# Performance work log

Hardware: AMD Instinct MI355X
Metric: run time of the kernel (lower is better)

Reference implementation:

```python
import jax, jax.numpy as jnp
import numpy as np

N_NODES = 50000
N_EDGES = 800000
N_GRAPHS = 512
IN_DIM, HID_DIM, LAT_DIM = 128, 128, 64


def _glorot(key, fan_in, fan_out):
    lim = np.sqrt(6.0 / (fan_in + fan_out))
    return jax.random.uniform(key, (fan_in, fan_out), jnp.float32, -lim, lim)


def gcn_conv(x, W, b, src, dst, deg_inv_sqrt):
    """PyG GCNConv: out = D^{-1/2}(A+I)D^{-1/2} x W + b (self-loops included)."""
    h = x @ W  # [N, F_out]
    norm = deg_inv_sqrt[src] * deg_inv_sqrt[dst]  # [E]
    msg = h[src] * norm[:, None]  # gather + scale, [E, F_out]
    out = jax.ops.segment_sum(msg, dst, num_segments=x.shape[0])  # scatter-add
    out = out + h * (deg_inv_sqrt * deg_inv_sqrt)[:, None]  # self-loop term
    return out + b


def setup_inputs() -> dict:
    key = jax.random.key(0)
    ks = jax.random.split(key, 12)
    x = jax.random.normal(ks[0], (N_NODES, IN_DIM), jnp.float32)
    edge_index = jax.random.randint(ks[1], (2, N_EDGES), 0, N_NODES, jnp.int64)
    batch = jnp.sort(jax.random.randint(ks[2], (N_NODES,), 0, N_GRAPHS, jnp.int64))
    return {
        "x": x,
        "edge_index": edge_index,
        "batch": batch,
        "W1": _glorot(ks[3], IN_DIM, HID_DIM), "b1": jnp.zeros((HID_DIM,), jnp.float32),
        "W2": _glorot(ks[4], HID_DIM, LAT_DIM), "b2": jnp.zeros((LAT_DIM,), jnp.float32),
        "W3": _glorot(ks[5], LAT_DIM, HID_DIM), "b3": jnp.zeros((HID_DIM,), jnp.float32),
        "W4": _glorot(ks[6], HID_DIM, IN_DIM), "b4": jnp.zeros((IN_DIM,), jnp.float32),
    }


def reference(x, edge_index, batch, W1, b1, W2, b2, W3, b3, W4, b4):
    n = x.shape[0]
    src, dst = edge_index[0], edge_index[1]
    # degrees with self-loops (PyG computes deg over col=dst, +1 for self-loop)
    deg = jax.ops.segment_sum(jnp.ones_like(dst, dtype=x.dtype), dst, num_segments=n) + 1.0
    dis = jax.lax.rsqrt(deg)
    # encoder
    h = jax.nn.relu(gcn_conv(x, W1, b1, src, dst, dis))
    z = gcn_conv(h, W2, b2, src, dst, dis)
    # scatter-mean pooling over graphs
    counts = jax.ops.segment_sum(jnp.ones((n,), x.dtype), batch, num_segments=N_GRAPHS)
    agg = jax.ops.segment_sum(z, batch, num_segments=N_GRAPHS) / jnp.maximum(counts, 1.0)[:, None]
    # decoder
    h2 = jax.nn.relu(gcn_conv(z, W3, b3, src, dst, dis))
    x_hat = gcn_conv(h2, W4, b4, src, dst, dis)
    return (x_hat, z, agg)
```

## Files before the change

### kernel.cpp

```cpp
#include <hip/hip_runtime.h>
#include <hip/hip_fp16.h>
#include <math.h>

#define N_NODES 50000
#define N_EDGES 800000
#define N_GRAPHS 512
#define CAP 62
#define NBINS 196
#define CAPB 5120
#define ABLK 1024

typedef unsigned short u16;
typedef unsigned int u32;
typedef __attribute__((ext_vector_type(8))) short bf16x8_t;
typedef __attribute__((ext_vector_type(4))) float f32x4_t;

constexpr int NBLK_A = (N_EDGES + ABLK - 1) / ABLK;

__device__ __forceinline__ u16 f2bf(float f) {
    u32 u = __builtin_bit_cast(u32, f);
    return (u16)((u + 0x7fffu + ((u >> 16) & 1u)) >> 16);
}
__device__ __forceinline__ float bf2f(u16 s) {
    return __builtin_bit_cast(float, (u32)s << 16);
}
__device__ __forceinline__ float bf_lo(u32 u) { return __builtin_bit_cast(float, u << 16); }
__device__ __forceinline__ float bf_hi(u32 u) { return __builtin_bit_cast(float, u & 0xffff0000u); }

__device__ __forceinline__ int block_exscan(int val, int* lds, int tid) {
    lds[tid] = val;
    __syncthreads();
#pragma unroll
    for (int off = 1; off < 256; off <<= 1) {
        int t = (tid >= off) ? lds[tid - off] : 0;
        __syncthreads();
        lds[tid] += t;
        __syncthreads();
    }
    return lds[tid] - val;
}

__global__ __launch_bounds__(256) void bin_scatter(const int* __restrict__ src,
                                                   const int* __restrict__ dst,
                                                   u32* __restrict__ binCnt,
                                                   u32* __restrict__ binList) {
    __shared__ int cur[NBINS];
    __shared__ int lsStart[NBINS];
    __shared__ int gbase[NBINS];
    __shared__ int scanbuf[256];
    __shared__ u32 stage[ABLK];
    __shared__ int gpos[ABLK];
    int t = threadIdx.x;
    int e0 = blockIdx.x * ABLK;
    int nEdge = min(ABLK, N_EDGES - e0);

    for (int i = t; i < NBINS; i += 256) cur[i] = 0;
    __syncthreads();

    int myBin[4], myRank[4];
    u32 myPack[4];
    int nmy = 0;
    if (t * 4 < nEdge) {
        nmy = 4;
        int4 dv = *reinterpret_cast<const int4*>(dst + e0 + t * 4);
        int4 sv = *reinterpret_cast<const int4*>(src + e0 + t * 4);
        int ds[4] = {dv.x, dv.y, dv.z, dv.w};
        int ss[4] = {sv.x, sv.y, sv.z, sv.w};
#pragma unroll
        for (int j = 0; j < 4; j++) {
            int d = ds[j];
            int bin = d >> 8;
            myBin[j] = bin;
            myPack[j] = (u32)(ss[j] & 0xFFFF) | ((u32)(d & 0xFF) << 16);
            myRank[j] = atomicAdd(&cur[bin], 1);
        }
    }
    __syncthreads();
    int v = (t < NBINS) ? cur[t] : 0;
    int ex = block_exscan(v, scanbuf, t);
    if (t < NBINS) {
        lsStart[t] = ex;
        gbase[t] = (v > 0) ? (int)atomicAdd(&binCnt[t * 16], (u32)v) : 0;
    }
    __syncthreads();
    for (int j = 0; j < nmy; j++) {
        int bin = myBin[j];
        int idx = lsStart[bin] + myRank[j];
        int p = gbase[bin] + myRank[j];
        stage[idx] = myPack[j];
        gpos[idx] = (p < CAPB) ? (bin * CAPB + p) : -1;
    }
    __syncthreads();
    for (int i = t; i < nEdge; i += 256) {
        int p = gpos[i];
        if (p >= 0) binList[p] = stage[i];
    }
}

__global__ __launch_bounds__(256) void bucket_build(const u32* __restrict__ binList,
                                                    const u32* __restrict__ binCnt,
                                                    u32* __restrict__ bucket,
                                                    float* __restrict__ dis) {
    __shared__ u32 rec[256 * 32];
    int b = blockIdx.x, t = threadIdx.x;
    for (int i = t; i < 256 * 32; i += 256) rec[i] = 0;
    __syncthreads();
    int ecnt = min((int)binCnt[b * 16], CAPB);
    const u32* lst = binList + (size_t)b * CAPB;
    u16* rec16 = reinterpret_cast<u16*>(rec);
    for (int i = t; i < ecnt; i += 256) {
        u32 pk = lst[i];
        int dlow = (pk >> 16) & 0xFF;
        int pos = (int)atomicAdd(&rec[dlow * 32], 1u);
        if (pos < CAP) rec16[dlow * 64 + 2 + pos] = (u16)(pk & 0xFFFF);
    }
    __syncthreads();
    int node0 = b * 256;
    int nNode = min(256, N_NODES - node0);
    for (int i = t; i < nNode * 32; i += 256)
        bucket[(size_t)node0 * 32 + i] = rec[i];
    if (t < nNode) dis[node0 + t] = 1.0f / sqrtf((float)rec[t * 32] + 1.0f);
}

__global__ void convert_x_bf16(const float* __restrict__ x, u16* __restrict__ xb) {
    int i = blockIdx.x * 256 + threadIdx.x;
    if (i >= (N_NODES * 128) / 4) return;
    float4 v = reinterpret_cast<const float4*>(x)[i];
    u32 lo = (u32)f2bf(v.x) | ((u32)f2bf(v.y) << 16);
    u32 hi = (u32)f2bf(v.z) | ((u32)f2bf(v.w) << 16);
    reinterpret_cast<uint2*>(xb)[i] = make_uint2(lo, hi);
}

__global__ void convert_wT_all(const float* __restrict__ W1, u16* __restrict__ wt1,
                               const float* __restrict__ W2, u16* __restrict__ wt2,
                               const float* __restrict__ W3, u16* __restrict__ wt3,
                               const float* __restrict__ W4, u16* __restrict__ wt4) {
    int idx = blockIdx.x * 256 + threadIdx.x;
    const float* Wf;
    u16* Wt;
    int K, N, off;
    if (idx < 16384)      { Wf = W1; Wt = wt1; K = 128; N = 128; off = 0; }
    else if (idx < 24576) { Wf = W2; Wt = wt2; K = 128; N = 64;  off = 16384; }
    else if (idx < 32768) { Wf = W3; Wt = wt3; K = 64;  N = 128; off = 24576; }
    else if (idx < 49152) { Wf = W4; Wt = wt4; K = 128; N = 128; off = 32768; }
    else return;
    int t = idx - off;
    int k = t / N, n = t % N;
    Wt[n * K + k] = f2bf(Wf[t]);
}

template <int N, int K, bool BIAS, bool RELU, bool SCALE>
__global__ __launch_bounds__(256) void gemm_mfma(const u16* __restrict__ A,
                                                 const u16* __restrict__ Wt,
                                                 const float* __restrict__ bias,
                                                 const float* __restrict__ dis,
                                                 u16* __restrict__ C) {
    constexpr int KB = K / 32;
    constexpr int TN = N / 64;
    constexpr int TM = (N_NODES + 63) / 64;
    int wave = threadIdx.x >> 6;
    int lane = threadIdx.x & 63;
    int W = blockIdx.x * 4 + wave;
    if (W >= TM * TN) return;
    int tm = W / TN, tn = W % TN;
    int r16 = lane & 15;
    int kg = lane >> 4;

    bf16x8_t bf[4][KB];
#pragma unroll
    for (int nr = 0; nr < 4; nr++) {
        int colg = tn * 64 + nr * 16 + r16;
#pragma unroll
        for (int kb = 0; kb < KB; kb++)
            bf[nr][kb] = *reinterpret_cast<const bf16x8_t*>(Wt + (size_t)colg * K + kb * 32 + kg * 8);
    }

    f32x4_t acc[4][4];
#pragma unroll
    for (int mr = 0; mr < 4; mr++)
#pragma unroll
        for (int nr = 0; nr < 4; nr++)
#pragma unroll
            for (int t = 0; t < 4; t++) acc[mr][nr][t] = 0.f;

#pragma unroll
    for (int mr = 0; mr < 4; mr++) {
        int row = tm * 64 + mr * 16 + r16;
        if (row >= N_NODES) row = N_NODES - 1;
        bf16x8_t af[KB];
#pragma unroll
        for (int kb = 0; kb < KB; kb++)
            af[kb] = *reinterpret_cast<const bf16x8_t*>(A + (size_t)row * K + kb * 32 + kg * 8);
#pragma unroll
        for (int kb = 0; kb < KB; kb++)
#pragma unroll
            for (int nr = 0; nr < 4; nr++)
                acc[mr][nr] = __builtin_amdgcn_mfma_f32_16x16x32_bf16(af[kb], bf[nr][kb],
                                                                      acc[mr][nr], 0, 0, 0);
    }

#pragma unroll
    for (int mr = 0; mr < 4; mr++) {
        float sc[4];
#pragma unroll
        for (int r = 0; r < 4; r++) {
            int row = tm * 64 + mr * 16 + kg * 4 + r;
            sc[r] = (SCALE && row < N_NODES) ? dis[row] : 1.f;
        }
#pragma unroll
        for (int nr = 0; nr < 4; nr++) {
            int colg = tn * 64 + nr * 16 + r16;
            float bv = BIAS ? bias[colg] : 0.f;
#pragma unroll
            for (int r = 0; r < 4; r++) {
                int row = tm * 64 + mr * 16 + kg * 4 + r;
                if (row < N_NODES) {
                    float v = acc[mr][nr][r] + bv;
                    if (RELU) v = fmaxf(v, 0.f);
                    if (SCALE) v *= sc[r];
                    C[(size_t)row * N + colg] = f2bf(v);
                }
            }
        }
    }
}

template <int F, bool RELU, bool BIAS, bool WF32, bool WBF16, bool SCALEOUT>
__global__ __launch_bounds__(256) void propagate_b(const u16* __restrict__ h,
                                                   const u32* __restrict__ bucket,
                                                   const float* __restrict__ dis,
                                                   const float* __restrict__ bias,
                                                   float* __restrict__ out_f,
                                                   u16* __restrict__ out_b) {
    int w = (blockIdx.x * blockDim.x + threadIdx.x) >> 6;
    int lane = threadIdx.x & 63;
    if (w >= N_NODES) return;
    const u32* bw = bucket + (size_t)w * 32;
    int deg = __builtin_amdgcn_readfirstlane(min((int)bw[0], CAP));
    const u16* slots = reinterpret_cast<const u16*>(bw) + 2;
    const u32* sw = reinterpret_cast<const u32*>(reinterpret_cast<const char*>(bw) + 4);
    float di = dis[w];

    if (F == 128) {
        const u32* hw = reinterpret_cast<const u32*>(h);
        float2 a0 = {0.f, 0.f}, a1 = {0.f, 0.f}, a2 = {0.f, 0.f}, a3 = {0.f, 0.f};
        int i = 0;
        for (; i + 16 <= deg; i += 16) {
            u32 cw[8], hv[16];
#pragma unroll
            for (int j = 0; j < 8; j++) cw[j] = sw[(i >> 1) + j];
#pragma unroll
            for (int j = 0; j < 8; j++) {
                hv[2 * j]     = hw[(size_t)(cw[j] & 0xffffu) * 64 + lane];
                hv[2 * j + 1] = hw[(size_t)(cw[j] >> 16) * 64 + lane];
            }
#pragma unroll
            for (int j = 0; j < 16; j++) {
                float lo = bf_lo(hv[j]), hi = bf_hi(hv[j]);
                if ((j & 3) == 0) { a0.x += lo; a0.y += hi; }
                else if ((j & 3) == 1) { a1.x += lo; a1.y += hi; }
                else if ((j & 3) == 2) { a2.x += lo; a2.y += hi; }
                else { a3.x += lo; a3.y += hi; }
            }
        }
        for (; i + 8 <= deg; i += 8) {
            u32 cw[4], hv[8];
#pragma unroll
            for (int j = 0; j < 4; j++) cw[j] = sw[(i >> 1) + j];
#pragma unroll
            for (int j = 0; j < 4; j++) {
                hv[2 * j]     = hw[(size_t)(cw[j] & 0xffffu) * 64 + lane];
                hv[2 * j + 1] = hw[(size_t)(cw[j] >> 16) * 64 + lane];
            }
#pragma unroll
            for (int j = 0; j < 8; j++) {
                float lo = bf_lo(hv[j]), hi = bf_hi(hv[j]);
                if ((j & 3) == 0) { a0.x += lo; a0.y += hi; }
                else if ((j & 3) == 1) { a1.x += lo; a1.y += hi; }
                else if ((j & 3) == 2) { a2.x += lo; a2.y += hi; }
                else { a3.x += lo; a3.y += hi; }
            }
        }
        for (; i < deg; i++) {
            u32 u = hw[(size_t)slots[i] * 64 + lane];
            a0.x += bf_lo(u);
            a0.y += bf_hi(u);
        }
        u32 su = hw[(size_t)w * 64 + lane];
        float ox = (a0.x + a1.x + a2.x + a3.x + bf_lo(su)) * di;
        float oy = (a0.y + a1.y + a2.y + a3.y + bf_hi(su)) * di;
        if (BIAS) {
            float2 bv = reinterpret_cast<const float2*>(bias)[lane];
            ox += bv.x;
            oy += bv.y;
        }
        if (RELU) { ox = fmaxf(ox, 0.f); oy = fmaxf(oy, 0.f); }
        if (WF32) {
            reinterpret_cast<float2*>(out_f + (size_t)w * 128)[lane] = make_float2(ox, oy);
        }
        if (WBF16) {
            float wx = SCALEOUT ? ox * di : ox;
            float wy = SCALEOUT ? oy * di : oy;
            u32 pk = (u32)f2bf(wx) | ((u32)f2bf(wy) << 16);
            reinterpret_cast<u32*>(out_b)[(size_t)w * 64 + lane] = pk;
        }
    } else {
        float a0 = 0.f, a1 = 0.f, a2 = 0.f, a3 = 0.f;
        int i = 0;
        for (; i + 16 <= deg; i += 16) {
            u32 cw[8];
            u16 hv[16];
#pragma unroll
            for (int j = 0; j < 8; j++) cw[j] = sw[(i >> 1) + j];
#pragma unroll
            for (int j = 0; j < 8; j++) {
                hv[2 * j]     = h[(size_t)(cw[j] & 0xffffu) * 64 + lane];
                hv[2 * j + 1] = h[(size_t)(cw[j] >> 16) * 64 + lane];
            }
#pragma unroll
            for (int j = 0; j < 16; j++) {
                float v = bf2f(hv[j]);
                if ((j & 3) == 0) a0 += v;
                else if ((j & 3) == 1) a1 += v;
                else if ((j & 3) == 2) a2 += v;
                else a3 += v;
            }
        }
        for (; i + 8 <= deg; i += 8) {
            u32 cw[4];
            u16 hv[8];
#pragma unroll
            for (int j = 0; j < 4; j++) cw[j] = sw[(i >> 1) + j];
#pragma unroll
            for (int j = 0; j < 4; j++) {
                hv[2 * j]     = h[(size_t)(cw[j] & 0xffffu) * 64 + lane];
                hv[2 * j + 1] = h[(size_t)(cw[j] >> 16) * 64 + lane];
            }
#pragma unroll
            for (int j = 0; j < 8; j++) {
                float v = bf2f(hv[j]);
                if ((j & 3) == 0) a0 += v;
                else if ((j & 3) == 1) a1 += v;
                else if ((j & 3) == 2) a2 += v;
                else a3 += v;
            }
        }
        for (; i < deg; i++) a0 += bf2f(h[(size_t)slots[i] * 64 + lane]);
        float o = (a0 + a1 + a2 + a3 + bf2f(h[(size_t)w * 64 + lane])) * di;
        if (BIAS) o += bias[lane];
        if (RELU) o = fmaxf(o, 0.f);
        if (WF32) out_f[(size_t)w * 64 + lane] = o;
        if (WBF16) out_b[(size_t)w * 64 + lane] = f2bf(SCALEOUT ? o * di : o);
    }
}

__global__ __launch_bounds__(256) void pool_kernel(const float* __restrict__ z,
                                                   const int* __restrict__ batch,
                                                   float* __restrict__ agg) {
    __shared__ float part[3][64];
    int g = blockIdx.x;
    int wave = threadIdx.x >> 6;
    int lane = threadIdx.x & 63;
    int l = 0, h = N_NODES;
    while (l < h) { int m = (l + h) >> 1; if (batch[m] < g) l = m + 1; else h = m; }
    int s = l;
    h = N_NODES;
    while (l < h) { int m = (l + h) >> 1; if (batch[m] < g + 1) l = m + 1; else h = m; }
    int e = l;
    float acc = 0.f;
    for (int i = s + wave; i < e; i += 4) acc += z[(size_t)i * 64 + lane];
    if (wave) part[wave - 1][lane] = acc;
    __syncthreads();
    if (wave == 0) {
        acc += part[0][lane] + part[1][lane] + part[2][lane];
        agg[(size_t)g * 64 + lane] = acc / fmaxf((float)(e - s), 1.0f);
    }
}

extern "C" void kernel_launch(void* const* d_in, const int* in_sizes, int n_in,
                              void* d_out, int out_size, void* d_ws, size_t ws_size,
                              hipStream_t stream) {
    const float* x   = (const float*)d_in[0];
    const int* eidx  = (const int*)d_in[1];
    const int* batch = (const int*)d_in[2];
    const float* W1  = (const float*)d_in[3];
    const float* b1  = (const float*)d_in[4];
    const float* W2  = (const float*)d_in[5];
    const float* b2  = (const float*)d_in[6];
    const float* W3  = (const float*)d_in[7];
    const float* b3  = (const float*)d_in[8];
    const float* W4  = (const float*)d_in[9];
    const float* b4  = (const float*)d_in[10];

    const int* src = eidx;
    const int* dst = eidx + N_EDGES;

    float* out_xhat = (float*)d_out;
    float* out_z    = out_xhat + (size_t)N_NODES * 128;
    float* out_agg  = out_z + (size_t)N_NODES * 64;

    char* p = (char*)d_ws;
    auto alloc = [&](size_t bytes) { char* r = p; p += (bytes + 255) & ~(size_t)255; return r; };
    u16* arena0 = (u16*)alloc((size_t)N_NODES * 128 * 2);
    u16* arena1 = (u16*)alloc((size_t)N_NODES * 128 * 2);
    u16* c1     = (u16*)alloc((size_t)N_NODES * 64 * 2);
    u16* c2     = (u16*)alloc((size_t)N_NODES * 64 * 2);
    u16* wt1    = (u16*)alloc(128 * 128 * 2);
    u16* wt2    = (u16*)alloc(128 * 64 * 2);
    u16* wt3    = (u16*)alloc(64 * 128 * 2);
    u16* wt4    = (u16*)alloc(128 * 128 * 2);
    u32* bucket = (u32*)alloc((size_t)N_NODES * 128);
    u32* binCnt = (u32*)alloc(NBINS * 16 * 4);
    u32* binList= (u32*)alloc((size_t)NBINS * CAPB * 4);
    float* dis  = (float*)alloc(N_NODES * 4);

    hipMemsetAsync(binCnt, 0, NBINS * 16 * 4, stream);
    bin_scatter<<<NBLK_A, 256, 0, stream>>>(src, dst, binCnt, binList);
    bucket_build<<<NBINS, 256, 0, stream>>>(binList, binCnt, bucket, dis);

    convert_x_bf16<<<(N_NODES * 128 / 4 + 255) / 256, 256, 0, stream>>>(x, arena0);
    convert_wT_all<<<(49152 + 255) / 256, 256, 0, stream>>>(W1, wt1, W2, wt2, W3, wt3, W4, wt4);

    const int PROP_GRID = (N_NODES + 3) / 4;
    const int G128 = ((N_NODES + 63) / 64 * 2 + 3) / 4;
    const int G64  = ((N_NODES + 63) / 64 * 1 + 3) / 4;

    gemm_mfma<128, 128, false, false, true><<<G128, 256, 0, stream>>>(arena0, wt1, nullptr, dis, arena1);
    propagate_b<128, true, true, false, true, false><<<PROP_GRID, 256, 0, stream>>>(
        arena1, bucket, dis, b1, nullptr, arena0);
    gemm_mfma<64, 128, false, false, true><<<G64, 256, 0, stream>>>(arena0, wt2, nullptr, dis, c1);
    propagate_b<64, false, true, true, true, true><<<PROP_GRID, 256, 0, stream>>>(
        c1, bucket, dis, b2, out_z, c2);
    pool_kernel<<<N_GRAPHS, 256, 0, stream>>>(out_z, batch, out_agg);
    propagate_b<64, false, false, false, true, false><<<PROP_GRID, 256, 0, stream>>>(
        c2, bucket, dis, nullptr, nullptr, c1);
    gemm_mfma<128, 64, true, true, false><<<G128, 256, 0, stream>>>(c1, wt3, b3, dis, arena1);
    gemm_mfma<128, 128, false, false, true><<<G128, 256, 0, stream>>>(arena1, wt4, nullptr, dis, arena0);
    propagate_b<128, false, true, true, false, false><<<PROP_GRID, 256, 0, stream>>>(
        arena0, bucket, dis, b4, out_xhat, nullptr);
}
```

Measured before the change: 267.0 us.

## Fuse x conversion into first GEMM, merge weight conversion, persistent propagate grid

Removes the separate fp32-to-bf16 conversion kernel for x by having the first GEMM load fp32 rows and convert them in registers. The weight-transpose conversion moves into extra blocks of the edge-binning kernel, saving a launch. The propagate kernels switch to a fixed grid of 2048 blocks with a grid-stride loop over nodes, and the bias load is hoisted out of that loop. This cuts launches and one full pass over x. The cost is that the first GEMM now reads twice as many bytes, and the fixed grid may balance load unevenly across nodes.

```diff
diff --git a/kernel.cpp b/kernel.cpp
--- a/kernel.cpp
+++ b/kernel.cpp
@@ -9,13 +9,17 @@
 #define NBINS 196
 #define CAPB 5120
 #define ABLK 1024
+#define PROP_BLOCKS 2048
+#define PROP_WAVES (PROP_BLOCKS * 4)
 
 typedef unsigned short u16;
 typedef unsigned int u32;
 typedef __attribute__((ext_vector_type(8))) short bf16x8_t;
 typedef __attribute__((ext_vector_type(4))) float f32x4_t;
+typedef __attribute__((ext_vector_type(4))) unsigned int u32x4_t;
 
 constexpr int NBLK_A = (N_EDGES + ABLK - 1) / ABLK;
+constexpr int NCW = (49152 + 255) / 256;
 
 __device__ __forceinline__ u16 f2bf(float f) {
     u32 u = __builtin_bit_cast(u32, f);
@@ -26,6 +30,17 @@
 }
 __device__ __forceinline__ float bf_lo(u32 u) { return __builtin_bit_cast(float, u << 16); }
 __device__ __forceinline__ float bf_hi(u32 u) { return __builtin_bit_cast(float, u & 0xffff0000u); }
+
+__device__ __forceinline__ bf16x8_t cvt8(const float* p) {
+    float4 a = *reinterpret_cast<const float4*>(p);
+    float4 b = *reinterpret_cast<const float4*>(p + 4);
+    u32x4_t w;
+    w.x = (u32)f2bf(a.x) | ((u32)f2bf(a.y) << 16);
+    w.y = (u32)f2bf(a.z) | ((u32)f2bf(a.w) << 16);
+    w.z = (u32)f2bf(b.x) | ((u32)f2bf(b.y) << 16);
+    w.w = (u32)f2bf(b.z) | ((u32)f2bf(b.w) << 16);
+    return __builtin_bit_cast(bf16x8_t, w);
+}
 
 __device__ __forceinline__ int block_exscan(int val, int* lds, int tid) {
     lds[tid] = val;
@@ -40,10 +55,14 @@
     return lds[tid] - val;
 }
 
-__global__ __launch_bounds__(256) void bin_scatter(const int* __restrict__ src,
+__global__ __launch_bounds__(256) void pre_scatter(const int* __restrict__ src,
                                                    const int* __restrict__ dst,
                                                    u32* __restrict__ binCnt,
-                                                   u32* __restrict__ binList) {
+                                                   u32* __restrict__ binList,
+                                                   const float* __restrict__ W1, u16* __restrict__ wt1,
+                                                   const float* __restrict__ W2, u16* __restrict__ wt2,
+                                                   const float* __restrict__ W3, u16* __restrict__ wt3,
+                                                   const float* __restrict__ W4, u16* __restrict__ wt4) {
     __shared__ int cur[NBINS];
     __shared__ int lsStart[NBINS];
     __shared__ int gbase[NBINS];
@@ -51,6 +70,20 @@
     __shared__ u32 stage[ABLK];
     __shared__ int gpos[ABLK];
     int t = threadIdx.x;
+    if (blockIdx.x >= NBLK_A) {
+        int idx = (blockIdx.x - NBLK_A) * 256 + t;
+        const float* Wf;
+        u16* Wt;
+        int K, N, off;
+        if (idx < 16384)      { Wf = W1; Wt = wt1; K = 128; N = 128; off = 0; }
+        else if (idx < 24576) { Wf = W2; Wt = wt2; K = 128; N = 64;  off = 16384; }
+        else if (idx < 32768) { Wf = W3; Wt = wt3; K = 64;  N = 128; off = 24576; }
+        else                  { Wf = W4; Wt = wt4; K = 128; N = 128; off = 32768; }
+        int q = idx - off;
+        int k = q / N, n = q % N;
+        Wt[n * K + k] = f2bf(Wf[q]);
+        return;
+    }
     int e0 = blockIdx.x * ABLK;
     int nEdge = min(ABLK, N_EDGES - e0);
 
@@ -122,35 +155,8 @@
     if (t < nNode) dis[node0 + t] = 1.0f / sqrtf((float)rec[t * 32] + 1.0f);
 }
 
-__global__ void convert_x_bf16(const float* __restrict__ x, u16* __restrict__ xb) {
-    int i = blockIdx.x * 256 + threadIdx.x;
-    if (i >= (N_NODES * 128) / 4) return;
-    float4 v = reinterpret_cast<const float4*>(x)[i];
-    u32 lo = (u32)f2bf(v.x) | ((u32)f2bf(v.y) << 16);
-    u32 hi = (u32)f2bf(v.z) | ((u32)f2bf(v.w) << 16);
-    reinterpret_cast<uint2*>(xb)[i] = make_uint2(lo, hi);
-}
-
-__global__ void convert_wT_all(const float* __restrict__ W1, u16* __restrict__ wt1,
-                               const float* __restrict__ W2, u16* __restrict__ wt2,
-                               const float* __restrict__ W3, u16* __restrict__ wt3,
-                               const float* __restrict__ W4, u16* __restrict__ wt4) {
-    int idx = blockIdx.x * 256 + threadIdx.x;
-    const float* Wf;
-    u16* Wt;
-    int K, N, off;
-    if (idx < 16384)      { Wf = W1; Wt = wt1; K = 128; N = 128; off = 0; }
-    else if (idx < 24576) { Wf = W2; Wt = wt2; K = 128; N = 64;  off = 16384; }
-    else if (idx < 32768) { Wf = W3; Wt = wt3; K = 64;  N = 128; off = 24576; }
-    else if (idx < 49152) { Wf = W4; Wt = wt4; K = 128; N = 128; off = 32768; }
-    else return;
-    int t = idx - off;
-    int k = t / N, n = t % N;
-    Wt[n * K + k] = f2bf(Wf[t]);
-}
-
-template <int N, int K, bool BIAS, bool RELU, bool SCALE>
-__global__ __launch_bounds__(256) void gemm_mfma(const u16* __restrict__ A,
+template <int N, int K, bool BIAS, bool RELU, bool SCALE, bool AF32>
+__global__ __launch_bounds__(256) void gemm_mfma(const void* __restrict__ Avp,
                                                  const u16* __restrict__ Wt,
                                                  const float* __restrict__ bias,
                                                  const float* __restrict__ dis,
@@ -189,8 +195,15 @@
         if (row >= N_NODES) row = N_NODES - 1;
         bf16x8_t af[KB];
 #pragma unroll
-        for (int kb = 0; kb < KB; kb++)
-            af[kb] = *reinterpret_cast<const bf16x8_t*>(A + (size_t)row * K + kb * 32 + kg * 8);
+        for (int kb = 0; kb < KB; kb++) {
+            if constexpr (AF32) {
+                const float* Af = (const float*)Avp;
+                af[kb] = cvt8(Af + (size_t)row * K + kb * 32 + kg * 8);
+            } else {
+                const u16* Ab = (const u16*)Avp;
+                af[kb] = *reinterpret_cast<const bf16x8_t*>(Ab + (size_t)row * K + kb * 32 + kg * 8);
+            }
+        }
 #pragma unroll
         for (int kb = 0; kb < KB; kb++)
 #pragma unroll
@@ -232,125 +245,128 @@
                                                    const float* __restrict__ bias,
                                                    float* __restrict__ out_f,
                                                    u16* __restrict__ out_b) {
-    int w = (blockIdx.x * blockDim.x + threadIdx.x) >> 6;
+    int wid = (blockIdx.x * 256 + threadIdx.x) >> 6;
     int lane = threadIdx.x & 63;
-    if (w >= N_NODES) return;
-    const u32* bw = bucket + (size_t)w * 32;
-    int deg = __builtin_amdgcn_readfirstlane(min((int)bw[0], CAP));
-    const u16* slots = reinterpret_cast<const u16*>(bw) + 2;
-    const u32* sw = reinterpret_cast<const u32*>(reinterpret_cast<const char*>(bw) + 4);
-    float di = dis[w];
-
-    if (F == 128) {
-        const u32* hw = reinterpret_cast<const u32*>(h);
-        float2 a0 = {0.f, 0.f}, a1 = {0.f, 0.f}, a2 = {0.f, 0.f}, a3 = {0.f, 0.f};
-        int i = 0;
-        for (; i + 16 <= deg; i += 16) {
-            u32 cw[8], hv[16];
-#pragma unroll
-            for (int j = 0; j < 8; j++) cw[j] = sw[(i >> 1) + j];
-#pragma unroll
-            for (int j = 0; j < 8; j++) {
-                hv[2 * j]     = hw[(size_t)(cw[j] & 0xffffu) * 64 + lane];
-                hv[2 * j + 1] = hw[(size_t)(cw[j] >> 16) * 64 + lane];
-            }
-#pragma unroll
-            for (int j = 0; j < 16; j++) {
-                float lo = bf_lo(hv[j]), hi = bf_hi(hv[j]);
-                if ((j & 3) == 0) { a0.x += lo; a0.y += hi; }
-                else if ((j & 3) == 1) { a1.x += lo; a1.y += hi; }
-                else if ((j & 3) == 2) { a2.x += lo; a2.y += hi; }
-                else { a3.x += lo; a3.y += hi; }
-            }
+    float2 bv2 = make_float2(0.f, 0.f);
+    float bv1 = 0.f;
+    if (BIAS) {
+        if (F == 128) bv2 = reinterpret_cast<const float2*>(bias)[lane];
+        else          bv1 = bias[lane];
+    }
+    for (int w = wid; w < N_NODES; w += PROP_WAVES) {
+        const u32* bw = bucket + (size_t)w * 32;
+        int deg = __builtin_amdgcn_readfirstlane(min((int)bw[0], CAP));
+        const u16* slots = reinterpret_cast<const u16*>(bw) + 2;
+        const u32* sw = reinterpret_cast<const u32*>(reinterpret_cast<const char*>(bw) + 4);
+        float di = dis[w];
+
+        if (F == 128) {
+            const u32* hw = reinterpret_cast<const u32*>(h);
+            float2 a0 = {0.f, 0.f}, a1 = {0.f, 0.f}, a2 = {0.f, 0.f}, a3 = {0.f, 0.f};
+            int i = 0;
+            for (; i + 16 <= deg; i += 16) {
+                u32 cw[8], hv[16];
+#pragma unroll
+                for (int j = 0; j < 8; j++) cw[j] = sw[(i >> 1) + j];
+#pragma unroll
+                for (int j = 0; j < 8; j++) {
+                    hv[2 * j]     = hw[(size_t)(cw[j] & 0xffffu) * 64 + lane];
+                    hv[2 * j + 1] = hw[(size_t)(cw[j] >> 16) * 64 + lane];
+                }
+#pragma unroll
+                for (int j = 0; j < 16; j++) {
+                    float lo = bf_lo(hv[j]), hi = bf_hi(hv[j]);
+                    if ((j & 3) == 0) { a0.x += lo; a0.y += hi; }
+                    else if ((j & 3) == 1) { a1.x += lo; a1.y += hi; }
+                    else if ((j & 3) == 2) { a2.x += lo; a2.y += hi; }
+                    else { a3.x += lo; a3.y += hi; }
+                }
+            }
+            for (; i + 8 <= deg; i += 8) {
+                u32 cw[4], hv[8];
+#pragma unroll
+                for (int j = 0; j < 4; j++) cw[j] = sw[(i >> 1) + j];
+#pragma unroll
+                for (int j = 0; j < 4; j++) {
+                    hv[2 * j]     = hw[(size_t)(cw[j] & 0xffffu) * 64 + lane];
+                    hv[2 * j + 1] = hw[(size_t)(cw[j] >> 16) * 64 + lane];
+                }
+#pragma unroll
+                for (int j = 0; j < 8; j++) {
+                    float lo = bf_lo(hv[j]), hi = bf_hi(hv[j]);
+                    if ((j & 3) == 0) { a0.x += lo; a0.y += hi; }
+                    else if ((j & 3) == 1) { a1.x += lo; a1.y += hi; }
+                    else if ((j & 3) == 2) { a2.x += lo; a2.y += hi; }
+                    else { a3.x += lo; a3.y += hi; }
+                }
+            }
+            for (; i < deg; i++) {
+                u32 u = hw[(size_t)slots[i] * 64 + lane];
+                a0.x += bf_lo(u);
+                a0.y += bf_hi(u);
+            }
+            u32 su = hw[(size_t)w * 64 + lane];
+            float ox = (a0.x + a1.x + a2.x + a3.x + bf_lo(su)) * di;
+            float oy = (a0.y + a1.y + a2.y + a3.y + bf_hi(su)) * di;
+            if (BIAS) { ox += bv2.x; oy += bv2.y; }
+            if (RELU) { ox = fmaxf(ox, 0.f); oy = fmaxf(oy, 0.f); }
+            if (WF32) {
+                reinterpret_cast<float2*>(out_f + (size_t)w * 128)[lane] = make_float2(ox, oy);
+            }
+            if (WBF16) {
+                float wx = SCALEOUT ? ox * di : ox;
+                float wy = SCALEOUT ? oy * di : oy;
+                u32 pk = (u32)f2bf(wx) | ((u32)f2bf(wy) << 16);
+                reinterpret_cast<u32*>(out_b)[(size_t)w * 64 + lane] = pk;
+            }
+        } else {
+            float a0 = 0.f, a1 = 0.f, a2 = 0.f, a3 = 0.f;
+            int i = 0;
+            for (; i + 16 <= deg; i += 16) {
+                u32 cw[8];
+                u16 hv[16];
+#pragma unroll
+                for (int j = 0; j < 8; j++) cw[j] = sw[(i >> 1) + j];
+#pragma unroll
+                for (int j = 0; j < 8; j++) {
+                    hv[2 * j]     = h[(size_t)(cw[j] & 0xffffu) * 64 + lane];
+                    hv[2 * j + 1] = h[(size_t)(cw[j] >> 16) * 64 + lane];
+                }
+#pragma unroll
+                for (int j = 0; j < 16; j++) {
+                    float v = bf2f(hv[j]);
+                    if ((j & 3) == 0) a0 += v;
+                    else if ((j & 3) == 1) a1 += v;
+                    else if ((j & 3) == 2) a2 += v;
+                    else a3 += v;
+                }
+            }
+            for (; i + 8 <= deg; i += 8) {
+                u32 cw[4];
+                u16 hv[8];
+#pragma unroll
+                for (int j = 0; j < 4; j++) cw[j] = sw[(i >> 1) + j];
+#pragma unroll
+                for (int j = 0; j < 4; j++) {
+                    hv[2 * j]     = h[(size_t)(cw[j] & 0xffffu) * 64 + lane];
+                    hv[2 * j + 1] = h[(size_t)(cw[j] >> 16) * 64 + lane];
+                }
+#pragma unroll
+                for (int j = 0; j < 8; j++) {
+                    float v = bf2f(hv[j]);
+                    if ((j & 3) == 0) a0 += v;
+                    else if ((j & 3) == 1) a1 += v;
+                    else if ((j & 3) == 2) a2 += v;
+                    else a3 += v;
+                }
+            }
+            for (; i < deg; i++) a0 += bf2f(h[(size_t)slots[i] * 64 + lane]);
+            float o = (a0 + a1 + a2 + a3 + bf2f(h[(size_t)w * 64 + lane])) * di;
+            if (BIAS) o += bv1;
+            if (RELU) o = fmaxf(o, 0.f);
+            if (WF32) out_f[(size_t)w * 64 + lane] = o;
+            if (WBF16) out_b[(size_t)w * 64 + lane] = f2bf(SCALEOUT ? o * di : o);
         }
-        for (; i + 8 <= deg; i += 8) {
-            u32 cw[4], hv[8];
-#pragma unroll
-            for (int j = 0; j < 4; j++) cw[j] = sw[(i >> 1) + j];
-#pragma unroll
-            for (int j = 0; j < 4; j++) {
-                hv[2 * j]     = hw[(size_t)(cw[j] & 0xffffu) * 64 + lane];
-                hv[2 * j + 1] = hw[(size_t)(cw[j] >> 16) * 64 + lane];
-            }
-#pragma unroll
-            for (int j = 0; j < 8; j++) {
-                float lo = bf_lo(hv[j]), hi = bf_hi(hv[j]);
-                if ((j & 3) == 0) { a0.x += lo; a0.y += hi; }
-                else if ((j & 3) == 1) { a1.x += lo; a1.y += hi; }
-                else if ((j & 3) == 2) { a2.x += lo; a2.y += hi; }
-                else { a3.x += lo; a3.y += hi; }
-            }
-        }
-        for (; i < deg; i++) {
-            u32 u = hw[(size_t)slots[i] * 64 + lane];
-            a0.x += bf_lo(u);
-            a0.y += bf_hi(u);
-        }
-        u32 su = hw[(size_t)w * 64 + lane];
-        float ox = (a0.x + a1.x + a2.x + a3.x + bf_lo(su)) * di;
-        float oy = (a0.y + a1.y + a2.y + a3.y + bf_hi(su)) * di;
-        if (BIAS) {
-            float2 bv = reinterpret_cast<const float2*>(bias)[lane];
-            ox += bv.x;
-            oy += bv.y;
-        }
-        if (RELU) { ox = fmaxf(ox, 0.f); oy = fmaxf(oy, 0.f); }
-        if (WF32) {
-            reinterpret_cast<float2*>(out_f + (size_t)w * 128)[lane] = make_float2(ox, oy);
-        }
-        if (WBF16) {
-            float wx = SCALEOUT ? ox * di : ox;
-            float wy = SCALEOUT ? oy * di : oy;
-            u32 pk = (u32)f2bf(wx) | ((u32)f2bf(wy) << 16);
-            reinterpret_cast<u32*>(out_b)[(size_t)w * 64 + lane] = pk;
-        }
-    } else {
-        float a0 = 0.f, a1 = 0.f, a2 = 0.f, a3 = 0.f;
-        int i = 0;
-        for (; i + 16 <= deg; i += 16) {
-            u32 cw[8];
-            u16 hv[16];
-#pragma unroll
-            for (int j = 0; j < 8; j++) cw[j] = sw[(i >> 1) + j];
-#pragma unroll
-            for (int j = 0; j < 8; j++) {
-                hv[2 * j]     = h[(size_t)(cw[j] & 0xffffu) * 64 + lane];
-                hv[2 * j + 1] = h[(size_t)(cw[j] >> 16) * 64 + lane];
-            }
-#pragma unroll
-            for (int j = 0; j < 16; j++) {
-                float v = bf2f(hv[j]);
-                if ((j & 3) == 0) a0 += v;
-                else if ((j & 3) == 1) a1 += v;
-                else if ((j & 3) == 2) a2 += v;
-                else a3 += v;
-            }
-        }
-        for (; i + 8 <= deg; i += 8) {
-            u32 cw[4];
-            u16 hv[8];
-#pragma unroll
-            for (int j = 0; j < 4; j++) cw[j] = sw[(i >> 1) + j];
-#pragma unroll
-            for (int j = 0; j < 4; j++) {
-                hv[2 * j]     = h[(size_t)(cw[j] & 0xffffu) * 64 + lane];
-                hv[2 * j + 1] = h[(size_t)(cw[j] >> 16) * 64 + lane];
-            }
-#pragma unroll
-            for (int j = 0; j < 8; j++) {
-                float v = bf2f(hv[j]);
-                if ((j & 3) == 0) a0 += v;
-                else if ((j & 3) == 1) a1 += v;
-                else if ((j & 3) == 2) a2 += v;
-                else a3 += v;
-            }
-        }
-        for (; i < deg; i++) a0 += bf2f(h[(size_t)slots[i] * 64 + lane]);
-        float o = (a0 + a1 + a2 + a3 + bf2f(h[(size_t)w * 64 + lane])) * di;
-        if (BIAS) o += bias[lane];
-        if (RELU) o = fmaxf(o, 0.f);
-        if (WF32) out_f[(size_t)w * 64 + lane] = o;
-        if (WBF16) out_b[(size_t)w * 64 + lane] = f2bf(SCALEOUT ? o * di : o);
     }
 }
 
@@ -415,27 +431,28 @@
     float* dis  = (float*)alloc(N_NODES * 4);
 
     hipMemsetAsync(binCnt, 0, NBINS * 16 * 4, stream);
-    bin_scatter<<<NBLK_A, 256, 0, stream>>>(src, dst, binCnt, binList);
+    pre_scatter<<<NBLK_A + NCW, 256, 0, stream>>>(src, dst, binCnt, binList,
+                                                  W1, wt1, W2, wt2, W3, wt3, W4, wt4);
     bucket_build<<<NBINS, 256, 0, stream>>>(binList, binCnt, bucket, dis);
 
-    convert_x_bf16<<<(N_NODES * 128 / 4 + 255) / 256, 256, 0, stream>>>(x, arena0);
-    convert_wT_all<<<(49152 + 255) / 256, 256, 0, stream>>>(W1, wt1, W2, wt2, W3, wt3, W4, wt4);
-
-    const int PROP_GRID = (N_NODES + 3) / 4;
     const int G128 = ((N_NODES + 63) / 64 * 2 + 3) / 4;
     const int G64  = ((N_NODES + 63) / 64 * 1 + 3) / 4;
 
-    gemm_mfma<128, 128, false, false, true><<<G128, 256, 0, stream>>>(arena0, wt1, nullptr, dis, arena1);
-    propagate_b<128, true, true, false, true, false><<<PROP_GRID, 256, 0, stream>>>(
+    gemm_mfma<128, 128, false, false, true, true><<<G128, 256, 0, stream>>>(
+        x, wt1, nullptr, dis, arena1);
+    propagate_b<128, true, true, false, true, false><<<PROP_BLOCKS, 256, 0, stream>>>(
         arena1, bucket, dis, b1, nullptr, arena0);
-    gemm_mfma<64, 128, false, false, true><<<G64, 256, 0, stream>>>(arena0, wt2, nullptr, dis, c1);
-    propagate_b<64, false, true, true, true, true><<<PROP_GRID, 256, 0, stream>>>(
+    gemm_mfma<64, 128, false, false, true, false><<<G64, 256, 0, stream>>>(
+        arena0, wt2, nullptr, dis, c1);
+    propagate_b<64, false, true, true, true, true><<<PROP_BLOCKS, 256, 0, stream>>>(
         c1, bucket, dis, b2, out_z, c2);
     pool_kernel<<<N_GRAPHS, 256, 0, stream>>>(out_z, batch, out_agg);
-    propagate_b<64, false, false, false, true, false><<<PROP_GRID, 256, 0, stream>>>(
+    propagate_b<64, false, false, false, true, false><<<PROP_BLOCKS, 256, 0, stream>>>(
         c2, bucket, dis, nullptr, nullptr, c1);
-    gemm_mfma<128, 64, true, true, false><<<G128, 256, 0, stream>>>(c1, wt3, b3, dis, arena1);
-    gemm_mfma<128, 128, false, false, true><<<G128, 256, 0, stream>>>(arena1, wt4, nullptr, dis, arena0);
-    propagate_b<128, false, true, true, false, false><<<PROP_GRID, 256, 0, stream>>>(
+    gemm_mfma<128, 64, true, true, false, false><<<G128, 256, 0, stream>>>(
+        c1, wt3, b3, dis, arena1);
+    gemm_mfma<128, 128, false, false, true, false><<<G128, 256, 0, stream>>>(
+        arena1, wt4, nullptr, dis, arena0);
+    propagate_b<128, false, true, true, false, false><<<PROP_BLOCKS, 256, 0, stream>>>(
         arena0, bucket, dis, b4, out_xhat, nullptr);
 }
```

New measurement: 258.1 us. -3.3%, faster.
